# Kernel optimization log

Hardware: AMD Instinct MI355X
Metric: run time of the kernel (lower is better)

## Reference

```python
import jax, jax.numpy as jnp
import numpy as np

N_NODES = 200000
N_EDGES = 6400000
N_GRAPHS = 1024
N_EMB = 1032
D = 16


def _gcn_conv(x, W, b, src, dst, n):
    # PyG GCNConv: h = x W; symmetric norm with self-loops; aggregate onto target (dst)
    h = x @ W
    deg = jax.ops.segment_sum(jnp.ones_like(dst, dtype=h.dtype), dst, num_segments=n) + 1.0
    dis = jax.lax.rsqrt(deg)
    norm = dis[src] * dis[dst]                      # [E]
    agg = jax.ops.segment_sum(h[src] * norm[:, None], dst, num_segments=n)
    agg = agg + h * (dis * dis)[:, None]            # self-loop term
    return agg + b


def _protein_embed(ids, edge_index, batch_ids, emb, W1, b1, W2, b2):
    n = ids.shape[0]
    x = emb[ids]                                    # embedding lookup [N, D]
    src, dst = edge_index[0], edge_index[1]
    h = jax.nn.relu(_gcn_conv(x, W1, b1, src, dst, n))
    h = _gcn_conv(h, W2, b2, src, dst, n)
    # global_mean_pool over graphs
    sums = jax.ops.segment_sum(h, batch_ids, num_segments=N_GRAPHS)
    cnt = jax.ops.segment_sum(jnp.ones((n,), h.dtype), batch_ids, num_segments=N_GRAPHS)
    return sums / jnp.maximum(cnt, 1.0)[:, None]    # [B, D]


def setup_inputs() -> dict:
    key = jax.random.key(0)
    ks = jax.random.split(key, 10)
    emb = jax.random.normal(ks[0], (N_EMB, D), jnp.float32) * 0.1
    W1 = jax.random.normal(ks[1], (D, D), jnp.float32) * (1.0 / np.sqrt(D))
    W2 = jax.random.normal(ks[2], (D, D), jnp.float32) * (1.0 / np.sqrt(D))
    fcW = jax.random.normal(ks[3], (6, 2 * D), jnp.float32) * (1.0 / np.sqrt(2 * D))
    b1 = jnp.zeros((D,), jnp.float32)
    b2 = jnp.zeros((D,), jnp.float32)
    fcb = jnp.zeros((6,), jnp.float32)
    rx = jax.random.randint(ks[4], (N_NODES,), 0, N_EMB)
    r_edge_index = jax.random.randint(ks[5], (2, N_EDGES), 0, N_NODES)
    r_batch = jnp.sort(jax.random.randint(ks[6], (N_NODES,), 0, N_GRAPHS))
    lx = jax.random.randint(ks[7], (N_NODES,), 0, N_EMB)
    l_edge_index = jax.random.randint(ks[8], (2, N_EDGES), 0, N_NODES)
    l_batch = jnp.sort(jax.random.randint(ks[9], (N_NODES,), 0, N_GRAPHS))
    return {"emb": emb, "W1": W1, "b1": b1, "W2": W2, "b2": b2, "fcW": fcW, "fcb": fcb,
            "rx": rx, "r_edge_index": r_edge_index, "r_batch": r_batch,
            "lx": lx, "l_edge_index": l_edge_index, "l_batch": l_batch}


def reference(emb, W1, b1, W2, b2, fcW, fcb, rx, r_edge_index, r_batch, lx, l_edge_index, l_batch):
    r = _protein_embed(rx, r_edge_index, r_batch, emb, W1, b1, W2, b2)
    l = _protein_embed(lx, l_edge_index, l_batch, emb, W1, b1, W2, b2)
    h = jnp.concatenate([r, l], axis=1)             # [B, 2D]
    out = h @ fcW.T + fcb                           # [B, 6]
    return out[:, :3], out[:, 3:]
```

## Files before the change

kernel.cpp:

```cpp
#include <hip/hip_runtime.h>
#include <hip/hip_bf16.h>

#define N_NODES 200000
#define N_GRAPHS 1024
#define D 16
#define NEDGE 6400000

#define BNODES 256
#define NBUK 782
#define NCH 512
#define ECHUNK 12500
#define OSTRIDE (NBUK + 1)
#define CAP 9216
#define GBLK 12500
#define GHALF 6250

__global__ __launch_bounds__(1024) void pA(
        const int* __restrict__ srcR, const int* __restrict__ dstR,
        const int* __restrict__ srcL, const int* __restrict__ dstL,
        unsigned int* __restrict__ slabC_R, unsigned int* __restrict__ slabC_L,
        int* __restrict__ offsT_R, int* __restrict__ offsT_L) {
    const int* src = blockIdx.y ? srcL : srcR;
    const int* dst = blockIdx.y ? dstL : dstR;
    unsigned int* slabC = blockIdx.y ? slabC_L : slabC_R;
    int* offsT = blockIdx.y ? offsT_L : offsT_R;

    __shared__ unsigned int stage[ECHUNK];
    __shared__ int lh[NBUK];
    __shared__ int lcur[NBUK];
    __shared__ int wsum[16];
    int t = threadIdx.x;
    int wave = t >> 6, lane = t & 63;
    int c = blockIdx.x;
    int base = c * ECHUNK;

    for (int k = t; k < NBUK; k += 1024) lh[k] = 0;
    __syncthreads();
    for (int e = t; e < ECHUNK; e += 1024)
        atomicAdd(&lh[((unsigned int)dst[base + e]) >> 8], 1);
    __syncthreads();

    int v = (t < NBUK) ? lh[t] : 0;
    int x = v;
#pragma unroll
    for (int d0 = 1; d0 < 64; d0 <<= 1) {
        int y = __shfl_up(x, d0, 64);
        if (lane >= d0) x += y;
    }
    if (lane == 63) wsum[wave] = x;
    __syncthreads();
    if (wave == 0 && lane < 16) {
        int s = wsum[lane];
#pragma unroll
        for (int d0 = 1; d0 < 16; d0 <<= 1) {
            int y = __shfl_up(s, d0, 64);
            if (lane >= d0) s += y;
        }
        wsum[lane] = s;
    }
    __syncthreads();
    int excl = x - v + (wave ? wsum[wave - 1] : 0);
    if (t < NBUK) lcur[t] = excl;
    __syncthreads();

    for (int e = t; e < ECHUNK; e += 1024) {
        int d = dst[base + e];
        int s = src[base + e];
        int pos = atomicAdd(&lcur[d >> 8], 1);
        stage[pos] = ((unsigned int)(d & 255) << 18) | (unsigned int)s;
    }
    __syncthreads();
    for (int e = t; e < ECHUNK; e += 1024) slabC[base + e] = stage[e];
    if (t < NBUK) offsT[c * OSTRIDE + t] = excl;
    if (t == 0) offsT[c * OSTRIDE + NBUK] = ECHUNK;
}

__global__ __launch_bounds__(256) void tr_kernel(
        const int* __restrict__ offsT_R, const int* __restrict__ offsT_L,
        int* __restrict__ offsTT_R, int* __restrict__ offsTT_L) {
    const int* in = blockIdx.z ? offsT_L : offsT_R;
    int* outp = blockIdx.z ? offsTT_L : offsTT_R;
    __shared__ int tile[32][33];
    int lx = threadIdx.x & 31, ly = threadIdx.x >> 5;
#pragma unroll
    for (int r = 0; r < 32; r += 8) {
        int row = blockIdx.y * 32 + ly + r;
        int col = blockIdx.x * 32 + lx;
        if (col < OSTRIDE) tile[ly + r][lx] = in[row * OSTRIDE + col];
    }
    __syncthreads();
#pragma unroll
    for (int r = 0; r < 32; r += 8) {
        int orow = blockIdx.x * 32 + ly + r;
        int ocol = blockIdx.y * 32 + lx;
        if (orow < OSTRIDE) outp[orow * NCH + ocol] = tile[lx][ly + r];
    }
}

__global__ __launch_bounds__(256) void pB(
        const unsigned int* __restrict__ slabC_R, const unsigned int* __restrict__ slabC_L,
        const int* __restrict__ offsTT_R, const int* __restrict__ offsTT_L,
        unsigned int* __restrict__ slabR, unsigned int* __restrict__ slabL,
        int2* __restrict__ metaR, int2* __restrict__ metaL,
        float* __restrict__ disR, float* __restrict__ disL) {
    int y = blockIdx.y;
    const unsigned int* slabC = y ? slabC_L : slabC_R;
    const int* offsTT = y ? offsTT_L : offsTT_R;
    unsigned int* slab = y ? slabL : slabR;
    int2* meta = y ? metaL : metaR;
    float* dis = y ? disL : disR;

    __shared__ unsigned int sin_[CAP];
    __shared__ unsigned int sout[CAP];
    __shared__ int hcnt[BNODES], hoff[BNODES], hcur[BNODES];
    __shared__ int wtot[4];
    __shared__ int totc;
    int t = threadIdx.x;
    int lane = t & 63, wave = t >> 6;
    int b = blockIdx.x;

    int a0 = offsTT[b * NCH + t],        e0 = offsTT[(b + 1) * NCH + t];
    int a1 = offsTT[b * NCH + t + 256],  e1 = offsTT[(b + 1) * NCH + t + 256];
    int len = (e0 - a0) + (e1 - a1);

    int x = len;
#pragma unroll
    for (int d0 = 1; d0 < 64; d0 <<= 1) {
        int yy = __shfl_up(x, d0, 64);
        if (lane >= d0) x += yy;
    }
    if (lane == 63) wtot[wave] = x;
    hcnt[t] = 0;
    __syncthreads();
    int pre = 0;
    for (int w2 = 0; w2 < wave; w2++) pre += wtot[w2];
    int sbase = x - len + pre;
    if (t == 255) totc = sbase + len;
    __syncthreads();

    int p = sbase;
    {
        int cb = t * ECHUNK;
        for (int i = (a0 & ~3); i < e0; i += 4) {
            uint4 v = *(const uint4*)(slabC + cb + i);
            unsigned int vv[4] = {v.x, v.y, v.z, v.w};
#pragma unroll
            for (int k = 0; k < 4; k++) {
                int idx = i + k;
                if (idx >= a0 && idx < e0) { if (p < CAP) sin_[p] = vv[k]; p++; }
            }
        }
        cb = (t + 256) * ECHUNK;
        for (int i = (a1 & ~3); i < e1; i += 4) {
            uint4 v = *(const uint4*)(slabC + cb + i);
            unsigned int vv[4] = {v.x, v.y, v.z, v.w};
#pragma unroll
            for (int k = 0; k < 4; k++) {
                int idx = i + k;
                if (idx >= a1 && idx < e1) { if (p < CAP) sin_[p] = vv[k]; p++; }
            }
        }
    }
    __syncthreads();
    int cnt = totc;
    if (cnt > CAP) cnt = CAP;

    for (int i = t; i < cnt; i += 256) atomicAdd(&hcnt[sin_[i] >> 18], 1);
    __syncthreads();

    int v2 = hcnt[t];
    int x2 = v2;
#pragma unroll
    for (int d0 = 1; d0 < 64; d0 <<= 1) {
        int yy = __shfl_up(x2, d0, 64);
        if (lane >= d0) x2 += yy;
    }
    if (lane == 63) wtot[wave] = x2;
    __syncthreads();
    int pre2 = 0;
    for (int w2 = 0; w2 < wave; w2++) pre2 += wtot[w2];
    int ex = x2 - v2 + pre2;
    hoff[t] = ex;
    hcur[t] = ex;
    __syncthreads();

    for (int i = t; i < cnt; i += 256) {
        unsigned int r = sin_[i];
        int pp = atomicAdd(&hcur[r >> 18], 1);
        if (pp < CAP) sout[pp] = r & 0x3FFFFu;
    }
    __syncthreads();

    int gb = b * CAP;
    for (int i = t; i < cnt; i += 256) slab[gb + i] = sout[i];
    int node = (b << 8) + t;
    if (node < N_NODES) {
        meta[node] = make_int2(gb + hoff[t], gb + hoff[t] + hcnt[t]);
        dis[node] = rsqrtf((float)hcnt[t] + 1.0f);
    }
}

__global__ __launch_bounds__(256) void t1_kernel(
        const int* __restrict__ idsR, const int* __restrict__ idsL,
        const float* __restrict__ emb, const float* __restrict__ W,
        const float* __restrict__ disR, const float* __restrict__ disL,
        __hip_bfloat16* __restrict__ hsR, __hip_bfloat16* __restrict__ hsL) {
    int y = blockIdx.y;
    const int* ids = y ? idsL : idsR;
    const float* dis = y ? disL : disR;
    __hip_bfloat16* hs = y ? hsL : hsR;
    __shared__ float sW[D][D];
    __shared__ float sx[16][D + 1];
    int t = threadIdx.x;
    int j = t & 15, g = t >> 4;
    sW[g][j] = W[t];
    int i = (blockIdx.x << 4) + g;
    sx[g][j] = emb[(size_t)ids[i] * D + j];
    __syncthreads();
    float acc = 0.f;
#pragma unroll
    for (int k = 0; k < D; k++) acc += sx[g][k] * sW[k][j];
    hs[(size_t)i * D + j] = __float2bfloat16(acc * dis[i]);
}

__global__ __launch_bounds__(256) void g1_kernel(
        const int2* __restrict__ metaR, const int2* __restrict__ metaL,
        const unsigned int* __restrict__ csrR, const unsigned int* __restrict__ csrL,
        const __hip_bfloat16* __restrict__ hs1R, const __hip_bfloat16* __restrict__ hs1L,
        const float* __restrict__ disR, const float* __restrict__ disL,
        const float* __restrict__ b1, const float* __restrict__ W2,
        __hip_bfloat16* __restrict__ hs2R, __hip_bfloat16* __restrict__ hs2L) {
    int half = (blockIdx.x >= GHALF);
    int bx = blockIdx.x - (half ? GHALF : 0);
    const int2* meta = half ? metaL : metaR;
    const unsigned int* csr = half ? csrL : csrR;
    const __hip_bfloat16* hs1 = half ? hs1L : hs1R;
    const float* dis = half ? disL : disR;
    __hip_bfloat16* hs2 = half ? hs2L : hs2R;

    __shared__ float sW[D][D];
    __shared__ float sx[32][D + 1];
    int t = threadIdx.x;
    int jp = t & 7, g = t >> 3;
    sW[t >> 4][t & 15] = W2[t];
    int i = (bx << 5) + g;
    int2 be = meta[i];
    float2 acc = __bfloat1622float2(
        *(const __hip_bfloat162*)(hs1 + (size_t)i * D + 2 * jp));
    int e = be.x, end = be.y;
    for (; e + 8 <= end; e += 8) {
        int my = (int)csr[e + jp];
#pragma unroll
        for (int n = 0; n < 8; n++) {
            int s = __shfl(my, n, 8);
            float2 f = __bfloat1622float2(
                *(const __hip_bfloat162*)(hs1 + (size_t)s * D + 2 * jp));
            acc.x += f.x; acc.y += f.y;
        }
    }
    for (; e < end; e++) {
        int s = csr[e];
        float2 f = __bfloat1622float2(
            *(const __hip_bfloat162*)(hs1 + (size_t)s * D + 2 * jp));
        acc.x += f.x; acc.y += f.y;
    }
    float di = dis[i];
    sx[g][2 * jp]     = fmaxf(acc.x * di + b1[2 * jp], 0.f);
    sx[g][2 * jp + 1] = fmaxf(acc.y * di + b1[2 * jp + 1], 0.f);
    __syncthreads();
    float a0 = 0.f, a1 = 0.f;
#pragma unroll
    for (int k = 0; k < D; k++) {
        float xv = sx[g][k];
        a0 += xv * sW[k][2 * jp];
        a1 += xv * sW[k][2 * jp + 1];
    }
    *(__hip_bfloat162*)(hs2 + (size_t)i * D + 2 * jp) =
        __float22bfloat162_rn(make_float2(a0 * di, a1 * di));
}

__global__ __launch_bounds__(256) void g2_kernel(
        const int2* __restrict__ metaR, const int2* __restrict__ metaL,
        const unsigned int* __restrict__ csrR, const unsigned int* __restrict__ csrL,
        const __hip_bfloat16* __restrict__ hs2R, const __hip_bfloat16* __restrict__ hs2L,
        const float* __restrict__ disR, const float* __restrict__ disL,
        const float* __restrict__ b2,
        const int* __restrict__ batR, const int* __restrict__ batL,
        float* __restrict__ sumsR, float* __restrict__ sumsL,
        float* __restrict__ cntR, float* __restrict__ cntL) {
    int half = (blockIdx.x >= GHALF);
    int bx = blockIdx.x - (half ? GHALF : 0);
    const int2* meta = half ? metaL : metaR;
    const unsigned int* csr = half ? csrL : csrR;
    const __hip_bfloat16* hs2 = half ? hs2L : hs2R;
    const float* dis = half ? disL : disR;
    const int* batch = half ? batL : batR;
    float* sums = half ? sumsL : sumsR;
    float* cnt = half ? cntL : cntR;

    __shared__ float sv[32][D + 1];
    __shared__ int sb[32];
    int t = threadIdx.x;
    int jp = t & 7, g = t >> 3;
    int i = (bx << 5) + g;
    int2 be = meta[i];
    float2 acc = __bfloat1622float2(
        *(const __hip_bfloat162*)(hs2 + (size_t)i * D + 2 * jp));
    int e = be.x, end = be.y;
    for (; e + 8 <= end; e += 8) {
        int my = (int)csr[e + jp];
#pragma unroll
        for (int n = 0; n < 8; n++) {
            int s = __shfl(my, n, 8);
            float2 f = __bfloat1622float2(
                *(const __hip_bfloat162*)(hs2 + (size_t)s * D + 2 * jp));
            acc.x += f.x; acc.y += f.y;
        }
    }
    for (; e < end; e++) {
        int s = csr[e];
        float2 f = __bfloat1622float2(
            *(const __hip_bfloat162*)(hs2 + (size_t)s * D + 2 * jp));
        acc.x += f.x; acc.y += f.y;
    }
    float di = dis[i];
    int bi = batch[i];
    sv[g][2 * jp]     = acc.x * di + b2[2 * jp];
    sv[g][2 * jp + 1] = acc.y * di + b2[2 * jp + 1];
    if (jp == 0) sb[g] = bi;
    __syncthreads();
    bool runend = (g == 31) || (sb[g + 1] != bi);
    if (runend) {
        float s0 = 0.f, s1 = 0.f;
        int gg = g;
        while (gg >= 0 && sb[gg] == bi) { s0 += sv[gg][2 * jp]; s1 += sv[gg][2 * jp + 1]; gg--; }
        atomicAdd(&sums[bi * D + 2 * jp], s0);
        atomicAdd(&sums[bi * D + 2 * jp + 1], s1);
        if (jp == 0) atomicAdd(&cnt[bi], (float)(g - gg));
    }
}

__global__ void final_kernel(const float* __restrict__ rs, const float* __restrict__ rc,
                             const float* __restrict__ ls, const float* __restrict__ lc,
                             const float* __restrict__ fcW, const float* __restrict__ fcb,
                             float* __restrict__ out) {
    int b = blockIdx.x * blockDim.x + threadIdx.x;
    if (b >= N_GRAPHS) return;
    float hc[2 * D];
    float rn = fmaxf(rc[b], 1.f), ln = fmaxf(lc[b], 1.f);
#pragma unroll
    for (int j = 0; j < D; j++) {
        hc[j]     = rs[b * D + j] / rn;
        hc[D + j] = ls[b * D + j] / ln;
    }
#pragma unroll
    for (int c = 0; c < 6; c++) {
        float acc = fcb[c];
#pragma unroll
        for (int j = 0; j < 2 * D; j++) acc += hc[j] * fcW[c * 2 * D + j];
        if (c < 3) out[b * 3 + c] = acc;
        else       out[N_GRAPHS * 3 + b * 3 + (c - 3)] = acc;
    }
}

extern "C" void kernel_launch(void* const* d_in, const int* in_sizes, int n_in,
                              void* d_out, int out_size, void* d_ws, size_t ws_size,
                              hipStream_t stream) {
    const float* emb = (const float*)d_in[0];
    const float* W1  = (const float*)d_in[1];
    const float* b1  = (const float*)d_in[2];
    const float* W2  = (const float*)d_in[3];
    const float* b2  = (const float*)d_in[4];
    const float* fcW = (const float*)d_in[5];
    const float* fcb = (const float*)d_in[6];
    const int* rx = (const int*)d_in[7];
    const int* re = (const int*)d_in[8];
    const int* rb = (const int*)d_in[9];
    const int* lx = (const int*)d_in[10];
    const int* le = (const int*)d_in[11];
    const int* lb = (const int*)d_in[12];
    float* out = (float*)d_out;

    char* w = (char*)d_ws;
    unsigned int* slabC_R = (unsigned int*)w;
    __hip_bfloat16* hs1R = (__hip_bfloat16*)w;
    __hip_bfloat16* hs1L = hs1R + (size_t)N_NODES * D;
    __hip_bfloat16* hs2R = hs1L + (size_t)N_NODES * D;
    __hip_bfloat16* hs2L = hs2R + (size_t)N_NODES * D;
    w += (size_t)NEDGE * 4;
    unsigned int* slabC_L = (unsigned int*)w;  w += (size_t)NEDGE * 4;
    unsigned int* slabR = (unsigned int*)w;    w += (size_t)NBUK * CAP * 4;
    unsigned int* slabL = (unsigned int*)w;    w += (size_t)NBUK * CAP * 4;
    int* offsT_R = (int*)w;                    w += (size_t)NCH * OSTRIDE * 4;
    int* offsT_L = (int*)w;                    w += (size_t)NCH * OSTRIDE * 4;
    int* offsTT_R = (int*)w;                   w += (size_t)OSTRIDE * NCH * 4;
    int* offsTT_L = (int*)w;                   w += (size_t)OSTRIDE * NCH * 4;
    int2* metaR = (int2*)w;                    w += (size_t)N_NODES * 8;
    int2* metaL = (int2*)w;                    w += (size_t)N_NODES * 8;
    float* disR = (float*)w;                   w += (size_t)N_NODES * 4;
    float* disL = (float*)w;                   w += (size_t)N_NODES * 4;
    float* sums0 = (float*)w;                  w += (size_t)N_GRAPHS * D * 4;
    float* cnt0  = (float*)w;                  w += (size_t)N_GRAPHS * 4;
    float* sums1 = (float*)w;                  w += (size_t)N_GRAPHS * D * 4;
    float* cnt1  = (float*)w;                  w += (size_t)N_GRAPHS * 4;

    const int* srcR = re;  const int* dstR = re + NEDGE;
    const int* srcL = le;  const int* dstL = le + NEDGE;

    hipMemsetAsync(sums0, 0, ((size_t)N_GRAPHS * (D + 1)) * 2 * sizeof(float), stream);

    pA<<<dim3(NCH, 2), 1024, 0, stream>>>(srcR, dstR, srcL, dstL,
                                          slabC_R, slabC_L, offsT_R, offsT_L);
    tr_kernel<<<dim3((OSTRIDE + 31) / 32, NCH / 32, 2), 256, 0, stream>>>(
        offsT_R, offsT_L, offsTT_R, offsTT_L);
    pB<<<dim3(NBUK, 2), 256, 0, stream>>>(slabC_R, slabC_L, offsTT_R, offsTT_L,
                                          slabR, slabL, metaR, metaL, disR, disL);

    t1_kernel<<<dim3(GBLK, 2), 256, 0, stream>>>(rx, lx, emb, W1, disR, disL, hs1R, hs1L);
    g1_kernel<<<2 * GHALF, 256, 0, stream>>>(metaR, metaL, slabR, slabL,
                                             hs1R, hs1L, disR, disL, b1, W2, hs2R, hs2L);
    g2_kernel<<<2 * GHALF, 256, 0, stream>>>(metaR, metaL, slabR, slabL,
                                             hs2R, hs2L, disR, disL, b2, rb, lb,
                                             sums0, sums1, cnt0, cnt1);
    final_kernel<<<(N_GRAPHS + 255) / 256, 256, 0, stream>>>(
        sums0, cnt0, sums1, cnt1, fcW, fcb, out);
}
```

Measured before the change: 534.7 us.

## Vectorize edge bucketing loads, write pB slab directly, interleave R/L blocks, nontemporal CSR

Edge bucketing in pA now reads src/dst as int4 and copies the staged buffer out as uint4, cutting the number of memory instructions. pB drops its shared-memory output staging and scatters node-sorted sources straight to global memory, which saves LDS and a barrier but makes the global writes uncoalesced. The gather kernels interleave R and L blocks by parity instead of splitting them into halves, and they read CSR indices with nontemporal loads to keep those streamed values from displacing the feature rows in cache.

```diff
diff --git a/kernel.cpp b/kernel.cpp
--- a/kernel.cpp
+++ b/kernel.cpp
@@ -10,10 +10,10 @@
 #define NBUK 782
 #define NCH 512
 #define ECHUNK 12500
+#define EC4 (ECHUNK / 4)
 #define OSTRIDE (NBUK + 1)
 #define CAP 9216
 #define GBLK 12500
-#define GHALF 6250
 
 __global__ __launch_bounds__(1024) void pA(
         const int* __restrict__ srcR, const int* __restrict__ dstR,
@@ -33,11 +33,18 @@
     int wave = t >> 6, lane = t & 63;
     int c = blockIdx.x;
     int base = c * ECHUNK;
+    const int4* dst4 = (const int4*)(dst + base);
+    const int4* src4 = (const int4*)(src + base);
 
     for (int k = t; k < NBUK; k += 1024) lh[k] = 0;
     __syncthreads();
-    for (int e = t; e < ECHUNK; e += 1024)
-        atomicAdd(&lh[((unsigned int)dst[base + e]) >> 8], 1);
+    for (int i = t; i < EC4; i += 1024) {
+        int4 d4 = dst4[i];
+        atomicAdd(&lh[((unsigned int)d4.x) >> 8], 1);
+        atomicAdd(&lh[((unsigned int)d4.y) >> 8], 1);
+        atomicAdd(&lh[((unsigned int)d4.z) >> 8], 1);
+        atomicAdd(&lh[((unsigned int)d4.w) >> 8], 1);
+    }
     __syncthreads();
 
     int v = (t < NBUK) ? lh[t] : 0;
@@ -63,14 +70,21 @@
     if (t < NBUK) lcur[t] = excl;
     __syncthreads();
 
-    for (int e = t; e < ECHUNK; e += 1024) {
-        int d = dst[base + e];
-        int s = src[base + e];
-        int pos = atomicAdd(&lcur[d >> 8], 1);
-        stage[pos] = ((unsigned int)(d & 255) << 18) | (unsigned int)s;
-    }
-    __syncthreads();
-    for (int e = t; e < ECHUNK; e += 1024) slabC[base + e] = stage[e];
+    for (int i = t; i < EC4; i += 1024) {
+        int4 d4 = dst4[i];
+        int4 s4 = src4[i];
+        int dd[4] = {d4.x, d4.y, d4.z, d4.w};
+        int ss[4] = {s4.x, s4.y, s4.z, s4.w};
+#pragma unroll
+        for (int k = 0; k < 4; k++) {
+            int pos = atomicAdd(&lcur[dd[k] >> 8], 1);
+            stage[pos] = ((unsigned int)(dd[k] & 255) << 18) | (unsigned int)ss[k];
+        }
+    }
+    __syncthreads();
+    uint4* out4 = (uint4*)(slabC + base);
+    const uint4* st4 = (const uint4*)stage;
+    for (int i = t; i < EC4; i += 1024) out4[i] = st4[i];
     if (t < NBUK) offsT[c * OSTRIDE + t] = excl;
     if (t == 0) offsT[c * OSTRIDE + NBUK] = ECHUNK;
 }
@@ -111,7 +125,6 @@
     float* dis = y ? disL : disR;
 
     __shared__ unsigned int sin_[CAP];
-    __shared__ unsigned int sout[CAP];
     __shared__ int hcnt[BNODES], hoff[BNODES], hcur[BNODES];
     __shared__ int wtot[4];
     __shared__ int totc;
@@ -184,15 +197,12 @@
     hcur[t] = ex;
     __syncthreads();
 
+    int gb = b * CAP;
     for (int i = t; i < cnt; i += 256) {
         unsigned int r = sin_[i];
         int pp = atomicAdd(&hcur[r >> 18], 1);
-        if (pp < CAP) sout[pp] = r & 0x3FFFFu;
-    }
-    __syncthreads();
-
-    int gb = b * CAP;
-    for (int i = t; i < cnt; i += 256) slab[gb + i] = sout[i];
+        if (pp < CAP) slab[gb + pp] = r & 0x3FFFFu;
+    }
     int node = (b << 8) + t;
     if (node < N_NODES) {
         meta[node] = make_int2(gb + hoff[t], gb + hoff[t] + hcnt[t]);
@@ -230,8 +240,8 @@
         const float* __restrict__ disR, const float* __restrict__ disL,
         const float* __restrict__ b1, const float* __restrict__ W2,
         __hip_bfloat16* __restrict__ hs2R, __hip_bfloat16* __restrict__ hs2L) {
-    int half = (blockIdx.x >= GHALF);
-    int bx = blockIdx.x - (half ? GHALF : 0);
+    int half = blockIdx.x & 1;
+    int bx = blockIdx.x >> 1;
     const int2* meta = half ? metaL : metaR;
     const unsigned int* csr = half ? csrL : csrR;
     const __hip_bfloat16* hs1 = half ? hs1L : hs1R;
@@ -249,7 +259,7 @@
         *(const __hip_bfloat162*)(hs1 + (size_t)i * D + 2 * jp));
     int e = be.x, end = be.y;
     for (; e + 8 <= end; e += 8) {
-        int my = (int)csr[e + jp];
+        int my = (int)__builtin_nontemporal_load(csr + e + jp);
 #pragma unroll
         for (int n = 0; n < 8; n++) {
             int s = __shfl(my, n, 8);
@@ -259,7 +269,7 @@
         }
     }
     for (; e < end; e++) {
-        int s = csr[e];
+        int s = (int)__builtin_nontemporal_load(csr + e);
         float2 f = __bfloat1622float2(
             *(const __hip_bfloat162*)(hs1 + (size_t)s * D + 2 * jp));
         acc.x += f.x; acc.y += f.y;
@@ -288,8 +298,8 @@
         const int* __restrict__ batR, const int* __restrict__ batL,
         float* __restrict__ sumsR, float* __restrict__ sumsL,
         float* __restrict__ cntR, float* __restrict__ cntL) {
-    int half = (blockIdx.x >= GHALF);
-    int bx = blockIdx.x - (half ? GHALF : 0);
+    int half = blockIdx.x & 1;
+    int bx = blockIdx.x >> 1;
     const int2* meta = half ? metaL : metaR;
     const unsigned int* csr = half ? csrL : csrR;
     const __hip_bfloat16* hs2 = half ? hs2L : hs2R;
@@ -308,7 +318,7 @@
         *(const __hip_bfloat162*)(hs2 + (size_t)i * D + 2 * jp));
     int e = be.x, end = be.y;
     for (; e + 8 <= end; e += 8) {
-        int my = (int)csr[e + jp];
+        int my = (int)__builtin_nontemporal_load(csr + e + jp);
 #pragma unroll
         for (int n = 0; n < 8; n++) {
             int s = __shfl(my, n, 8);
@@ -318,7 +328,7 @@
         }
     }
     for (; e < end; e++) {
-        int s = csr[e];
+        int s = (int)__builtin_nontemporal_load(csr + e);
         float2 f = __bfloat1622float2(
             *(const __hip_bfloat162*)(hs2 + (size_t)s * D + 2 * jp));
         acc.x += f.x; acc.y += f.y;
@@ -417,11 +427,11 @@
                                           slabR, slabL, metaR, metaL, disR, disL);
 
     t1_kernel<<<dim3(GBLK, 2), 256, 0, stream>>>(rx, lx, emb, W1, disR, disL, hs1R, hs1L);
-    g1_kernel<<<2 * GHALF, 256, 0, stream>>>(metaR, metaL, slabR, slabL,
-                                             hs1R, hs1L, disR, disL, b1, W2, hs2R, hs2L);
-    g2_kernel<<<2 * GHALF, 256, 0, stream>>>(metaR, metaL, slabR, slabL,
-                                             hs2R, hs2L, disR, disL, b2, rb, lb,
-                                             sums0, sums1, cnt0, cnt1);
+    g1_kernel<<<GBLK, 256, 0, stream>>>(metaR, metaL, slabR, slabL,
+                                        hs1R, hs1L, disR, disL, b1, W2, hs2R, hs2L);
+    g2_kernel<<<GBLK, 256, 0, stream>>>(metaR, metaL, slabR, slabL,
+                                        hs2R, hs2L, disR, disL, b2, rb, lb,
+                                        sums0, sums1, cnt0, cnt1);
     final_kernel<<<(N_GRAPHS + 255) / 256, 256, 0, stream>>>(
         sums0, cnt0, sums1, cnt1, fcW, fcb, out);
 }
```

Result: slower. 571.9 us (+7.0%).
